# Kernel tuning notes

Hardware: AMD Instinct MI355X
Metric: run time of the kernel (lower is better)

## Reference

```python
import jax, jax.numpy as jnp
import numpy as np

N_NODES = 50000
N_EDGES = 800000
N_EVAL = 500000
D = 96


def _sage_conv(x, edge_index, W_l, W_r, b):
    # PyG SAGEConv with aggr='add':
    #   aggr_out[v] = sum_{(u->v) in edges} x[u]
    #   out = aggr_out @ W_l^T-equivalent + b + x @ W_r  (we store W as [in, out])
    src, dst = edge_index[0], edge_index[1]
    msgs = x[src]                                        # [E, d_in] irregular gather
    aggr = jax.ops.segment_sum(msgs, dst, num_segments=x.shape[0])  # [N, d_in]
    return aggr @ W_l + b + x @ W_r                      # [N, d_out]


def setup_inputs() -> dict:
    key = jax.random.key(0)
    ks = jax.random.split(key, 8)
    scale = 1.0 / np.sqrt(D)
    Features = jax.random.normal(ks[0], (N_NODES, D), dtype=jnp.float32)
    A = jax.random.randint(ks[1], (2, N_EDGES), 0, N_NODES, dtype=jnp.int64)
    E = jax.random.randint(ks[2], (2, N_EVAL), 0, N_NODES, dtype=jnp.int64)
    W1_l = jax.random.normal(ks[3], (D, D), dtype=jnp.float32) * scale
    W1_r = jax.random.normal(ks[4], (D, D), dtype=jnp.float32) * scale
    b1 = jnp.zeros((D,), dtype=jnp.float32)
    W2_l = jax.random.normal(ks[5], (D, D), dtype=jnp.float32) * scale
    W2_r = jax.random.normal(ks[6], (D, D), dtype=jnp.float32) * scale
    b2 = jnp.zeros((D,), dtype=jnp.float32)
    return {"Features": Features, "A": A, "E": E,
            "W1_l": W1_l, "W1_r": W1_r, "b1": b1,
            "W2_l": W2_l, "W2_r": W2_r, "b2": b2}


def reference(Features, A, E, W1_l, W1_r, b1, W2_l, W2_r, b2):
    h = _sage_conv(Features, A, W1_l, W1_r, b1)          # [N, hidden]
    h = jax.nn.relu(h)
    # dropout in eval mode = identity
    h = _sage_conv(h, A, W2_l, W2_r, b2)                 # [N, out]
    # edge scoring: gather src/dst embeddings, dot, sigmoid
    src = h[E[0]]                                        # [n_eval, out]
    dst = h[E[1]]                                        # [n_eval, out]
    return jax.nn.sigmoid(jnp.sum(src * dst, axis=-1))   # [n_eval]
```

## Files before the change

kernel.cpp:

```cpp
#include <hip/hip_runtime.h>
#include <math.h>

#define N_NODES 50000
#define N_EDGES 800000
#define N_EVAL  500000
#define CSTRIDE 16
#define MAXDEG  64
#define NB_GEMM ((N_NODES + 63) / 64)
#define NB_AGG  ((N_NODES * 24 + 255) / 256)

__device__ __forceinline__ float4 f4add(float4 a, float4 b) {
    return make_float4(a.x + b.x, a.y + b.y, a.z + b.z, a.w + b.w);
}
__device__ __forceinline__ float4 f4fma(float s, float4 w, float4 a) {
    return make_float4(fmaf(s, w.x, a.x), fmaf(s, w.y, a.y),
                       fmaf(s, w.z, a.z), fmaf(s, w.w, a.w));
}


__device__ __forceinline__ void bucket_role(int idx, const int* __restrict__ src,
                                            const int* __restrict__ dst,
                                            int* __restrict__ degS,
                                            int* __restrict__ bucket) {
    int t = idx * 256 + threadIdx.x;
    if (t < N_EDGES / 4) {
        int4 s = ((const int4*)src)[t];
        int4 d = ((const int4*)dst)[t];
        int r0 = atomicAdd(&degS[(size_t)d.x * CSTRIDE], 1);
        int r1 = atomicAdd(&degS[(size_t)d.y * CSTRIDE], 1);
        int r2 = atomicAdd(&degS[(size_t)d.z * CSTRIDE], 1);
        int r3 = atomicAdd(&degS[(size_t)d.w * CSTRIDE], 1);
        if (r0 < MAXDEG) bucket[d.x * MAXDEG + r0] = s.x;
        if (r1 < MAXDEG) bucket[d.y * MAXDEG + r1] = s.y;
        if (r2 < MAXDEG) bucket[d.z * MAXDEG + r2] = s.z;
        if (r3 < MAXDEG) bucket[d.w * MAXDEG + r3] = s.w;
    }
}

__device__ __forceinline__ void aggr_role(int idx, const float* __restrict__ x,
                                          const int* __restrict__ degS,
                                          const int* __restrict__ bucket,
                                          float* __restrict__ out) {
    int gt = idx * 256 + threadIdx.x;
    if (gt >= N_NODES * 24) return;
    int v = gt / 24;
    int c = gt - v * 24;
    const float* xp = x + c * 4;
    const int* bk = bucket + v * MAXDEG;
    int deg = degS[(size_t)v * CSTRIDE];
    if (deg > MAXDEG) deg = MAXDEG;
    float4 a0 = make_float4(0.f, 0.f, 0.f, 0.f);
    float4 a1 = make_float4(0.f, 0.f, 0.f, 0.f);
    int i = 0;
    for (; i + 8 <= deg; i += 8) {
        int u0 = bk[i + 0], u1 = bk[i + 1], u2 = bk[i + 2], u3 = bk[i + 3];
        int u4 = bk[i + 4], u5 = bk[i + 5], u6 = bk[i + 6], u7 = bk[i + 7];
        float4 t0 = *(const float4*)(xp + (size_t)u0 * 96);
        float4 t1 = *(const float4*)(xp + (size_t)u1 * 96);
        float4 t2 = *(const float4*)(xp + (size_t)u2 * 96);
        float4 t3 = *(const float4*)(xp + (size_t)u3 * 96);
        float4 t4 = *(const float4*)(xp + (size_t)u4 * 96);
        float4 t5 = *(const float4*)(xp + (size_t)u5 * 96);
        float4 t6 = *(const float4*)(xp + (size_t)u6 * 96);
        float4 t7 = *(const float4*)(xp + (size_t)u7 * 96);
        a0 = f4add(a0, f4add(f4add(t0, t2), f4add(t4, t6)));
        a1 = f4add(a1, f4add(f4add(t1, t3), f4add(t5, t7)));
    }
    for (; i < deg; ++i) {
        int u = bk[i];
        a0 = f4add(a0, *(const float4*)(xp + (size_t)u * 96));
    }
    *(float4*)(out + (size_t)v * 96 + c * 4) = f4add(a0, a1);
}

__device__ __forceinline__ void selfgemm_role(int g, const float* __restrict__ X,
                                              const float* __restrict__ W96,
                                              const float* __restrict__ bias,
                                              float* __restrict__ S,
                                              float* __restrict__ Ws,
                                              float* __restrict__ xT) {
    const int tid = threadIdx.x;
    const int j   = tid & 31;
    const int ty  = tid >> 5;
    const int v0  = g * 64;

    float acc[8][3];
    float b0 = bias[j], b1 = bias[j + 32], b2 = bias[j + 64];
    #pragma unroll
    for (int r = 0; r < 8; ++r) { acc[r][0] = b0; acc[r][1] = b1; acc[r][2] = b2; }

    const int sr = tid >> 2;
    const int sc = tid & 3;
    int sv = v0 + sr; if (sv >= N_NODES) sv = N_NODES - 1;

    for (int kc = 0; kc < 3; ++kc) {
        const float* W = W96 + kc * (32 * 96);
        const int kbase = kc * 32;
        __syncthreads();
        #pragma unroll
        for (int i = 0; i < 3; ++i) {
            int f = tid + i * 256;
            *(float4*)(Ws + f * 4) = *(const float4*)(W + f * 4);
        }
        {
            const float* rowp = X + (size_t)sv * 96 + kbase;
            float4 a = *(const float4*)(rowp + sc * 4);
            float4 b = *(const float4*)(rowp + sc * 4 + 16);
            int k0 = sc * 4;
            xT[(k0 + 0) * 68 + sr] = a.x;
            xT[(k0 + 1) * 68 + sr] = a.y;
            xT[(k0 + 2) * 68 + sr] = a.z;
            xT[(k0 + 3) * 68 + sr] = a.w;
            xT[(k0 + 16) * 68 + sr] = b.x;
            xT[(k0 + 17) * 68 + sr] = b.y;
            xT[(k0 + 18) * 68 + sr] = b.z;
            xT[(k0 + 19) * 68 + sr] = b.w;
        }
        __syncthreads();
        #pragma unroll 8
        for (int kk = 0; kk < 32; ++kk) {
            float w0 = Ws[kk * 96 + j];
            float w1 = Ws[kk * 96 + j + 32];
            float w2 = Ws[kk * 96 + j + 64];
            float4 xa = *(const float4*)(xT + kk * 68 + ty * 8);
            float4 xb = *(const float4*)(xT + kk * 68 + ty * 8 + 4);
#define ROWFMA(r, xv)                                   \
            acc[r][0] = fmaf(xv, w0, acc[r][0]);        \
            acc[r][1] = fmaf(xv, w1, acc[r][1]);        \
            acc[r][2] = fmaf(xv, w2, acc[r][2]);
            ROWFMA(0, xa.x) ROWFMA(1, xa.y) ROWFMA(2, xa.z) ROWFMA(3, xa.w)
            ROWFMA(4, xb.x) ROWFMA(5, xb.y) ROWFMA(6, xb.z) ROWFMA(7, xb.w)
#undef ROWFMA
        }
    }
    #pragma unroll
    for (int r = 0; r < 8; ++r) {
        int v = v0 + ty * 8 + r;
        if (v < N_NODES) {
            S[(size_t)v * 96 + j]      = acc[r][0];
            S[(size_t)v * 96 + j + 32] = acc[r][1];
            S[(size_t)v * 96 + j + 64] = acc[r][2];
        }
    }
}


__global__ __launch_bounds__(256) void k_fusedA(const int* __restrict__ src,
                                                const int* __restrict__ dst,
                                                int* __restrict__ degS,
                                                int* __restrict__ bucket,
                                                const float* __restrict__ X,
                                                const float* __restrict__ Wr,
                                                const float* __restrict__ bias,
                                                float* __restrict__ S) {
    __shared__ float Ws[32 * 96];
    __shared__ float xT[32 * 68];
    int b = blockIdx.x;
    if (b & 1) selfgemm_role(b >> 1, X, Wr, bias, S, Ws, xT);
    else       bucket_role(b >> 1, src, dst, degS, bucket);
}

__global__ __launch_bounds__(256) void k_aggr(const float* __restrict__ x,
                                              const int* __restrict__ degS,
                                              const int* __restrict__ bucket,
                                              float* __restrict__ out) {
    aggr_role(blockIdx.x, x, degS, bucket, out);
}

__global__ __launch_bounds__(256) void k_fusedC(const float* __restrict__ h1,
                                                const int* __restrict__ degS,
                                                const int* __restrict__ bucket,
                                                float* __restrict__ aggrOut,
                                                const float* __restrict__ Wr,
                                                const float* __restrict__ bias,
                                                float* __restrict__ S) {
    __shared__ float Ws[32 * 96];
    __shared__ float xT[32 * 68];
    int b = blockIdx.x;
    int g = b / 7, r = b % 7;
    if (r == 3) {
        if (g < NB_GEMM) selfgemm_role(g, h1, Wr, bias, S, Ws, xT);
    } else {
        int idx = g * 6 + (r < 3 ? r : r - 1);
        if (idx < NB_AGG) aggr_role(idx, h1, degS, bucket, aggrOut);
    }
}

template <int RELU>
__global__ __launch_bounds__(192) void k_gemmH(const float* __restrict__ P,
                                               const float* __restrict__ Wl,
                                               const float* __restrict__ S,
                                               float* __restrict__ out) {
    __shared__ float Ws[32 * 96];
    __shared__ float xT[32 * 68];
    const int tid = threadIdx.x;
    const int q   = tid % 24;
    const int rg  = tid / 24;
    const int v0  = blockIdx.x * 64;

    const int  row0 = tid >> 3,         qd0 = tid & 7;
    const int  row1 = (tid + 192) >> 3, qd1 = (tid + 192) & 7;
    const int  row2 = (tid + 384) >> 3, qd2 = (tid + 384) & 7;
    const bool has2 = (tid < 128);
    int sv0 = v0 + row0; if (sv0 >= N_NODES) sv0 = N_NODES - 1;
    int sv1 = v0 + row1; if (sv1 >= N_NODES) sv1 = N_NODES - 1;
    int sv2 = v0 + row2; if (sv2 >= N_NODES) sv2 = N_NODES - 1;

    float4 acc[8];
    #pragma unroll
    for (int r = 0; r < 8; ++r) acc[r] = make_float4(0.f, 0.f, 0.f, 0.f);

    float4 wreg0, wreg1, wreg2, wreg3;
    float4 xreg0, xreg1, xreg2;

    auto load_chunk = [&](int kc) {
        const float* W = Wl + kc * (32 * 96);
        const int kbase = kc * 32;
        wreg0 = *(const float4*)(W + (tid + 0 * 192) * 4);
        wreg1 = *(const float4*)(W + (tid + 1 * 192) * 4);
        wreg2 = *(const float4*)(W + (tid + 2 * 192) * 4);
        wreg3 = *(const float4*)(W + (tid + 3 * 192) * 4);
        xreg0 = *(const float4*)(P + (size_t)sv0 * 96 + kbase + qd0 * 4);
        xreg1 = *(const float4*)(P + (size_t)sv1 * 96 + kbase + qd1 * 4);
        if (has2) xreg2 = *(const float4*)(P + (size_t)sv2 * 96 + kbase + qd2 * 4);
    };
    auto store_chunk = [&]() {
        *(float4*)(Ws + (tid + 0 * 192) * 4) = wreg0;
        *(float4*)(Ws + (tid + 1 * 192) * 4) = wreg1;
        *(float4*)(Ws + (tid + 2 * 192) * 4) = wreg2;
        *(float4*)(Ws + (tid + 3 * 192) * 4) = wreg3;
        int k0 = qd0 * 4;
        xT[(k0 + 0) * 68 + row0] = xreg0.x;
        xT[(k0 + 1) * 68 + row0] = xreg0.y;
        xT[(k0 + 2) * 68 + row0] = xreg0.z;
        xT[(k0 + 3) * 68 + row0] = xreg0.w;
        int k1 = qd1 * 4;
        xT[(k1 + 0) * 68 + row1] = xreg1.x;
        xT[(k1 + 1) * 68 + row1] = xreg1.y;
        xT[(k1 + 2) * 68 + row1] = xreg1.z;
        xT[(k1 + 3) * 68 + row1] = xreg1.w;
        if (has2) {
            int k2 = qd2 * 4;
            xT[(k2 + 0) * 68 + row2] = xreg2.x;
            xT[(k2 + 1) * 68 + row2] = xreg2.y;
            xT[(k2 + 2) * 68 + row2] = xreg2.z;
            xT[(k2 + 3) * 68 + row2] = xreg2.w;
        }
    };

    load_chunk(0);
    for (int kc = 0; kc < 3; ++kc) {
        __syncthreads();
        store_chunk();
        if (kc < 2) load_chunk(kc + 1);
        __syncthreads();
        #pragma unroll 8
        for (int kk = 0; kk < 32; ++kk) {
            float4 w  = *(const float4*)(Ws + kk * 96 + q * 4);
            float4 xa = *(const float4*)(xT + kk * 68 + rg * 8);
            float4 xb = *(const float4*)(xT + kk * 68 + rg * 8 + 4);
            acc[0] = f4fma(xa.x, w, acc[0]);
            acc[1] = f4fma(xa.y, w, acc[1]);
            acc[2] = f4fma(xa.z, w, acc[2]);
            acc[3] = f4fma(xa.w, w, acc[3]);
            acc[4] = f4fma(xb.x, w, acc[4]);
            acc[5] = f4fma(xb.y, w, acc[5]);
            acc[6] = f4fma(xb.z, w, acc[6]);
            acc[7] = f4fma(xb.w, w, acc[7]);
        }
    }
    #pragma unroll
    for (int r = 0; r < 8; ++r) {
        int v = v0 + rg * 8 + r;
        if (v < N_NODES) {
            float4 s4 = *(const float4*)(S + (size_t)v * 96 + q * 4);
            float4 o = f4add(acc[r], s4);
            if (RELU) {
                o.x = fmaxf(o.x, 0.f); o.y = fmaxf(o.y, 0.f);
                o.z = fmaxf(o.z, 0.f); o.w = fmaxf(o.w, 0.f);
            }
            *(float4*)(out + (size_t)v * 96 + q * 4) = o;
        }
    }
}

__global__ __launch_bounds__(256) void k_score(const float* __restrict__ h,
                                               const int* __restrict__ E,
                                               float* __restrict__ out) {
    int t = blockIdx.x * 256 + threadIdx.x;
    int e = t >> 3, sub = t & 7;
    if (e >= N_EVAL) return;
    int s = E[e];
    int d = E[N_EVAL + e];
    const float* ps = h + (size_t)s * 96 + sub * 12;
    const float* pd = h + (size_t)d * 96 + sub * 12;
    float dot = 0.f;
    #pragma unroll
    for (int i = 0; i < 3; ++i) {
        float4 a = *(const float4*)(ps + i * 4);
        float4 b = *(const float4*)(pd + i * 4);
        dot += a.x * b.x + a.y * b.y + a.z * b.z + a.w * b.w;
    }
    dot += __shfl_xor(dot, 1, 64);
    dot += __shfl_xor(dot, 2, 64);
    dot += __shfl_xor(dot, 4, 64);
    if (sub == 0) out[e] = 1.f / (1.f + expf(-dot));
}


extern "C" void kernel_launch(void* const* d_in, const int* in_sizes, int n_in,
                              void* d_out, int out_size, void* d_ws, size_t ws_size,
                              hipStream_t stream) {
    const float* Features = (const float*)d_in[0];
    const int*   A        = (const int*)d_in[1];
    const int*   E        = (const int*)d_in[2];
    const float* W1l = (const float*)d_in[3];
    const float* W1r = (const float*)d_in[4];
    const float* b1  = (const float*)d_in[5];
    const float* W2l = (const float*)d_in[6];
    const float* W2r = (const float*)d_in[7];
    const float* b2  = (const float*)d_in[8];
    float* out = (float*)d_out;

    char* p = (char*)d_ws;
    auto alloc = [&](size_t bytes) -> char* {
        char* q = p;
        p += (bytes + 255) & ~(size_t)255;
        return q;
    };
    int*   degS   = (int*)alloc((size_t)N_NODES * CSTRIDE * 4);
    int*   bucket = (int*)alloc((size_t)N_NODES * MAXDEG * 4);
    float* bufA   = (float*)alloc((size_t)N_NODES * 96 * 4);
    float* bufB   = (float*)alloc((size_t)N_NODES * 96 * 4);
    float* bufS   = (float*)alloc((size_t)N_NODES * 96 * 4);

    const int* Asrc = A;
    const int* Adst = A + N_EDGES;

    hipMemsetAsync(degS, 0, (size_t)N_NODES * CSTRIDE * 4, stream);

    k_fusedA<<<2 * NB_GEMM, 256, 0, stream>>>(Asrc, Adst, degS, bucket,
                                              Features, W1r, b1, bufS);
    k_aggr<<<NB_AGG, 256, 0, stream>>>(Features, degS, bucket, bufA);
    k_gemmH<1><<<NB_GEMM, 192, 0, stream>>>(bufA, W1l, bufS, bufB);
    k_fusedC<<<7 * NB_GEMM, 256, 0, stream>>>(bufB, degS, bucket, bufA,
                                              W2r, b2, bufS);
    k_gemmH<0><<<NB_GEMM, 192, 0, stream>>>(bufA, W2l, bufS, bufA);
    k_score<<<(N_EVAL * 8 + 255) / 256, 256, 0, stream>>>(bufA, E, out);
}
```

Measured before the change: 309.5 us.

## Fuse layer-2 self and neighbor GEMMs into one K=192 pass; rebalance bucket blocks

For the second SAGE layer, the mixed aggregation+self-GEMM kernel is replaced by a plain aggregation kernel followed by one GEMM. That GEMM streams the aggregated features against W_l and then the layer input against W_r over six 32-wide K chunks, with register-prefetched shared-memory staging. This removes the write and re-read of the intermediate self-term buffer, but it gives up running the self-GEMM concurrently with the gather-heavy aggregation. Separately, the first fused kernel now uses two int2-based bucket-fill blocks per GEMM block instead of one int4-based block, spreading the atomic bucketing across more blocks.

```diff
diff --git a/kernel.cpp b/kernel.cpp
--- a/kernel.cpp
+++ b/kernel.cpp
@@ -18,22 +18,18 @@
 }
 
 
-__device__ __forceinline__ void bucket_role(int idx, const int* __restrict__ src,
-                                            const int* __restrict__ dst,
-                                            int* __restrict__ degS,
-                                            int* __restrict__ bucket) {
+__device__ __forceinline__ void bucket_role2(int idx, const int* __restrict__ src,
+                                             const int* __restrict__ dst,
+                                             int* __restrict__ degS,
+                                             int* __restrict__ bucket) {
     int t = idx * 256 + threadIdx.x;
-    if (t < N_EDGES / 4) {
-        int4 s = ((const int4*)src)[t];
-        int4 d = ((const int4*)dst)[t];
+    if (t < N_EDGES / 2) {
+        int2 s = ((const int2*)src)[t];
+        int2 d = ((const int2*)dst)[t];
         int r0 = atomicAdd(&degS[(size_t)d.x * CSTRIDE], 1);
         int r1 = atomicAdd(&degS[(size_t)d.y * CSTRIDE], 1);
-        int r2 = atomicAdd(&degS[(size_t)d.z * CSTRIDE], 1);
-        int r3 = atomicAdd(&degS[(size_t)d.w * CSTRIDE], 1);
         if (r0 < MAXDEG) bucket[d.x * MAXDEG + r0] = s.x;
         if (r1 < MAXDEG) bucket[d.y * MAXDEG + r1] = s.y;
-        if (r2 < MAXDEG) bucket[d.z * MAXDEG + r2] = s.z;
-        if (r3 < MAXDEG) bucket[d.w * MAXDEG + r3] = s.w;
     }
 }
 
@@ -156,8 +152,13 @@
     __shared__ float Ws[32 * 96];
     __shared__ float xT[32 * 68];
     int b = blockIdx.x;
-    if (b & 1) selfgemm_role(b >> 1, X, Wr, bias, S, Ws, xT);
-    else       bucket_role(b >> 1, src, dst, degS, bucket);
+    int g = b / 3, r = b % 3;
+    if (r == 1) {
+        if (g < NB_GEMM) selfgemm_role(g, X, Wr, bias, S, Ws, xT);
+    } else {
+        int idx = g * 2 + (r == 0 ? 0 : 1);
+        bucket_role2(idx, src, dst, degS, bucket);
+    }
 }
 
 __global__ __launch_bounds__(256) void k_aggr(const float* __restrict__ x,
@@ -165,25 +166,6 @@
                                               const int* __restrict__ bucket,
                                               float* __restrict__ out) {
     aggr_role(blockIdx.x, x, degS, bucket, out);
-}
-
-__global__ __launch_bounds__(256) void k_fusedC(const float* __restrict__ h1,
-                                                const int* __restrict__ degS,
-                                                const int* __restrict__ bucket,
-                                                float* __restrict__ aggrOut,
-                                                const float* __restrict__ Wr,
-                                                const float* __restrict__ bias,
-                                                float* __restrict__ S) {
-    __shared__ float Ws[32 * 96];
-    __shared__ float xT[32 * 68];
-    int b = blockIdx.x;
-    int g = b / 7, r = b % 7;
-    if (r == 3) {
-        if (g < NB_GEMM) selfgemm_role(g, h1, Wr, bias, S, Ws, xT);
-    } else {
-        int idx = g * 6 + (r < 3 ? r : r - 1);
-        if (idx < NB_AGG) aggr_role(idx, h1, degS, bucket, aggrOut);
-    }
 }
 
 template <int RELU>
@@ -284,6 +266,107 @@
     }
 }
 
+template <int RELU>
+__global__ __launch_bounds__(192) void k_gemm(const float* __restrict__ P,
+                                              const float* __restrict__ X,
+                                              const float* __restrict__ Wl,
+                                              const float* __restrict__ Wr,
+                                              const float* __restrict__ bias,
+                                              float* __restrict__ out) {
+    __shared__ float Ws[32 * 96];
+    __shared__ float xT[32 * 68];
+    const int tid = threadIdx.x;
+    const int q   = tid % 24;
+    const int rg  = tid / 24;
+    const int v0  = blockIdx.x * 64;
+
+    const int  row0 = tid >> 3,         qd0 = tid & 7;
+    const int  row1 = (tid + 192) >> 3, qd1 = (tid + 192) & 7;
+    const int  row2 = (tid + 384) >> 3, qd2 = (tid + 384) & 7;
+    const bool has2 = (tid < 128);
+    int sv0 = v0 + row0; if (sv0 >= N_NODES) sv0 = N_NODES - 1;
+    int sv1 = v0 + row1; if (sv1 >= N_NODES) sv1 = N_NODES - 1;
+    int sv2 = v0 + row2; if (sv2 >= N_NODES) sv2 = N_NODES - 1;
+
+    float4 bv = *(const float4*)(bias + q * 4);
+    float4 acc[8];
+    #pragma unroll
+    for (int r = 0; r < 8; ++r) acc[r] = make_float4(0.f, 0.f, 0.f, 0.f);
+
+    float4 wreg0, wreg1, wreg2, wreg3;
+    float4 xreg0, xreg1, xreg2;
+
+    auto load_chunk = [&](int kc) {
+        const float* W = (kc < 3 ? Wl : Wr) + (kc % 3) * (32 * 96);
+        const float* M = (kc < 3 ? P : X);
+        const int kbase = (kc % 3) * 32;
+        wreg0 = *(const float4*)(W + (tid + 0 * 192) * 4);
+        wreg1 = *(const float4*)(W + (tid + 1 * 192) * 4);
+        wreg2 = *(const float4*)(W + (tid + 2 * 192) * 4);
+        wreg3 = *(const float4*)(W + (tid + 3 * 192) * 4);
+        xreg0 = *(const float4*)(M + (size_t)sv0 * 96 + kbase + qd0 * 4);
+        xreg1 = *(const float4*)(M + (size_t)sv1 * 96 + kbase + qd1 * 4);
+        if (has2) xreg2 = *(const float4*)(M + (size_t)sv2 * 96 + kbase + qd2 * 4);
+    };
+    auto store_chunk = [&]() {
+        *(float4*)(Ws + (tid + 0 * 192) * 4) = wreg0;
+        *(float4*)(Ws + (tid + 1 * 192) * 4) = wreg1;
+        *(float4*)(Ws + (tid + 2 * 192) * 4) = wreg2;
+        *(float4*)(Ws + (tid + 3 * 192) * 4) = wreg3;
+        int k0 = qd0 * 4;
+        xT[(k0 + 0) * 68 + row0] = xreg0.x;
+        xT[(k0 + 1) * 68 + row0] = xreg0.y;
+        xT[(k0 + 2) * 68 + row0] = xreg0.z;
+        xT[(k0 + 3) * 68 + row0] = xreg0.w;
+        int k1 = qd1 * 4;
+        xT[(k1 + 0) * 68 + row1] = xreg1.x;
+        xT[(k1 + 1) * 68 + row1] = xreg1.y;
+        xT[(k1 + 2) * 68 + row1] = xreg1.z;
+        xT[(k1 + 3) * 68 + row1] = xreg1.w;
+        if (has2) {
+            int k2 = qd2 * 4;
+            xT[(k2 + 0) * 68 + row2] = xreg2.x;
+            xT[(k2 + 1) * 68 + row2] = xreg2.y;
+            xT[(k2 + 2) * 68 + row2] = xreg2.z;
+            xT[(k2 + 3) * 68 + row2] = xreg2.w;
+        }
+    };
+
+    load_chunk(0);
+    for (int kc = 0; kc < 6; ++kc) {
+        __syncthreads();
+        store_chunk();
+        if (kc < 5) load_chunk(kc + 1);
+        __syncthreads();
+        #pragma unroll 8
+        for (int kk = 0; kk < 32; ++kk) {
+            float4 w  = *(const float4*)(Ws + kk * 96 + q * 4);
+            float4 xa = *(const float4*)(xT + kk * 68 + rg * 8);
+            float4 xb = *(const float4*)(xT + kk * 68 + rg * 8 + 4);
+            acc[0] = f4fma(xa.x, w, acc[0]);
+            acc[1] = f4fma(xa.y, w, acc[1]);
+            acc[2] = f4fma(xa.z, w, acc[2]);
+            acc[3] = f4fma(xa.w, w, acc[3]);
+            acc[4] = f4fma(xb.x, w, acc[4]);
+            acc[5] = f4fma(xb.y, w, acc[5]);
+            acc[6] = f4fma(xb.z, w, acc[6]);
+            acc[7] = f4fma(xb.w, w, acc[7]);
+        }
+    }
+    #pragma unroll
+    for (int r = 0; r < 8; ++r) {
+        int v = v0 + rg * 8 + r;
+        if (v < N_NODES) {
+            float4 o = f4add(acc[r], bv);
+            if (RELU) {
+                o.x = fmaxf(o.x, 0.f); o.y = fmaxf(o.y, 0.f);
+                o.z = fmaxf(o.z, 0.f); o.w = fmaxf(o.w, 0.f);
+            }
+            *(float4*)(out + (size_t)v * 96 + q * 4) = o;
+        }
+    }
+}
+
 __global__ __launch_bounds__(256) void k_score(const float* __restrict__ h,
                                                const int* __restrict__ E,
                                                float* __restrict__ out) {
@@ -339,12 +422,11 @@
 
     hipMemsetAsync(degS, 0, (size_t)N_NODES * CSTRIDE * 4, stream);
 
-    k_fusedA<<<2 * NB_GEMM, 256, 0, stream>>>(Asrc, Adst, degS, bucket,
+    k_fusedA<<<3 * NB_GEMM, 256, 0, stream>>>(Asrc, Adst, degS, bucket,
                                               Features, W1r, b1, bufS);
     k_aggr<<<NB_AGG, 256, 0, stream>>>(Features, degS, bucket, bufA);
     k_gemmH<1><<<NB_GEMM, 192, 0, stream>>>(bufA, W1l, bufS, bufB);
-    k_fusedC<<<7 * NB_GEMM, 256, 0, stream>>>(bufB, degS, bucket, bufA,
-                                              W2r, b2, bufS);
-    k_gemmH<0><<<NB_GEMM, 192, 0, stream>>>(bufA, W2l, bufS, bufA);
+    k_aggr<<<NB_AGG, 256, 0, stream>>>(bufB, degS, bucket, bufA);
+    k_gemm<0><<<NB_GEMM, 192, 0, stream>>>(bufA, bufB, W2l, W2r, b2, bufA);
     k_score<<<(N_EVAL * 8 + 255) / 256, 256, 0, stream>>>(bufA, E, out);
 }
```

After: 323.2 us. +4.4%, slower.
